# Performance work log

Hardware: AMD Instinct MI355X
Metric: run time of the kernel (lower is better)

## Reference

```python
import jax, jax.numpy as jnp
import numpy as np

N = 50000
E = 800000


def setup_inputs() -> dict:
    key = jax.random.key(0)
    ks = jax.random.split(key, 12)
    d, pd, h, md, od = 64, 3, 128, 64, 64

    def glorot(k, shape):
        fan_in = shape[0]
        return jax.random.normal(k, shape, dtype=jnp.float32) / jnp.sqrt(jnp.float32(fan_in))

    return {
        "x": jax.random.normal(ks[0], (N, d), dtype=jnp.float32),
        "pos": jax.random.normal(ks[1], (N, pd), dtype=jnp.float32),
        "edge_index": jax.random.randint(ks[2], (2, E), 0, N, dtype=jnp.int64 if jax.config.jax_enable_x64 else jnp.int32),
        "W1": glorot(ks[3], (2 * d + pd, h)),
        "b1": jnp.zeros((h,), dtype=jnp.float32),
        "W2": glorot(ks[4], (h, md)),
        "b2": jnp.zeros((md,), dtype=jnp.float32),
        "W3": glorot(ks[5], (d + md, h)),
        "b3": jnp.zeros((h,), dtype=jnp.float32),
        "W4": glorot(ks[6], (h, od)),
        "b4": jnp.zeros((od,), dtype=jnp.float32),
    }


def reference(x, pos, edge_index, W1, b1, W2, b2, W3, b3, W4, b4):
    # flow='target_to_source': i = edge_index[0] (aggregation node), j = edge_index[1]
    idx_i = edge_index[0]
    idx_j = edge_index[1]

    x_i = x[idx_i]          # [E, d]
    x_j = x[idx_j]          # [E, d]
    rel_pos = pos[idx_j] - pos[idx_i]  # [E, pd]  (neighbor_loc='position')

    # message MLP
    msg_in = jnp.concatenate([x_i, x_j - x_i, rel_pos], axis=1)  # [E, 2d+pd]
    hmsg = jax.nn.relu(msg_in @ W1 + b1)
    msg = hmsg @ W2 + b2  # [E, md]

    # scatter-mean aggregation at node i
    num_nodes = x.shape[0]
    summed = jax.ops.segment_sum(msg, idx_i, num_segments=num_nodes)  # [N, md]
    counts = jax.ops.segment_sum(jnp.ones((msg.shape[0],), dtype=msg.dtype), idx_i, num_segments=num_nodes)
    aggr = summed / jnp.maximum(counts, 1.0)[:, None]

    # update MLP (self_val=True: concat own features)
    upd_in = jnp.concatenate([x, aggr], axis=1)  # [N, d+md]
    hupd = jax.nn.relu(upd_in @ W3 + b3)
    return hupd @ W4 + b4  # [N, od]
```

## Files before the change

### kernel.cpp

```cpp
#include <hip/hip_runtime.h>


#define EPB 128
#define NPB 64

typedef __attribute__((ext_vector_type(8))) short bf16x8;
typedef __attribute__((ext_vector_type(4))) float f32x4;

static __device__ __forceinline__ unsigned short f2bf(float f) {
    union { float f; unsigned u; } v; v.f = f;
    unsigned u = v.u + 0x7FFFu + ((v.u >> 16) & 1u);
    return (unsigned short)(u >> 16);
}
static __device__ __forceinline__ float bf2f(unsigned short h) {
    union { unsigned u; float f; } v; v.u = ((unsigned)h) << 16;
    return v.f;
}


__global__ __launch_bounds__(256) void count_kernel(
    const int* __restrict__ ei0, int* __restrict__ cnt, int E)
{
    int e = blockIdx.x * 256 + threadIdx.x;
    if (e < E) atomicAdd(&cnt[ei0[e]], 1);
}

__global__ __launch_bounds__(1024) void scanA_kernel(
    const int* __restrict__ cnt, int* __restrict__ bsum, int N)
{
    __shared__ int ws[16];
    const int i = blockIdx.x * 1024 + threadIdx.x;
    int v = (i < N) ? cnt[i] : 0;
    #pragma unroll
    for (int d = 32; d >= 1; d >>= 1) v += __shfl_down(v, d, 64);
    if ((threadIdx.x & 63) == 0) ws[threadIdx.x >> 6] = v;
    __syncthreads();
    if (threadIdx.x == 0) {
        int s = 0;
        #pragma unroll
        for (int k = 0; k < 16; ++k) s += ws[k];
        bsum[blockIdx.x] = s;
    }
}

__global__ __launch_bounds__(1024) void scanC_kernel(
    const int* __restrict__ cnt, const int* __restrict__ bsum,
    int* __restrict__ off, int N, int Etot)
{
    __shared__ int wsum[16];
    __shared__ int boffs;
    const int i = blockIdx.x * 1024 + threadIdx.x;
    const int lane = threadIdx.x & 63, w = threadIdx.x >> 6;
    if (threadIdx.x < 64) {
        int acc = 0;
        for (int k = threadIdx.x; k < blockIdx.x; k += 64) acc += bsum[k];
        #pragma unroll
        for (int d = 32; d >= 1; d >>= 1) acc += __shfl_down(acc, d, 64);
        if (threadIdx.x == 0) boffs = acc;
    }
    const int v = (i < N) ? cnt[i] : 0;
    int incl = v;
    #pragma unroll
    for (int d = 1; d < 64; d <<= 1) {
        int t = __shfl_up(incl, d, 64);
        if (lane >= d) incl += t;
    }
    if (lane == 63) wsum[w] = incl;
    __syncthreads();
    int pre = 0;
    for (int k = 0; k < w; ++k) pre += wsum[k];
    if (i < N) off[i] = boffs + pre + incl - v;
    if (blockIdx.x == 0 && threadIdx.x == 0) off[N] = Etot;
}

__global__ __launch_bounds__(256) void fill_kernel(
    const int* __restrict__ ei0, const int* __restrict__ ei1,
    const int* __restrict__ off, int* __restrict__ cur,
    int2* __restrict__ eij, int E)
{
    int e = blockIdx.x * 256 + threadIdx.x;
    if (e < E) {
        const int i = ei0[e];
        const int p = atomicAdd(&cur[i], 1);
        int2 v; v.x = i; v.y = ei1[e];
        eij[off[i] + p] = v;
    }
}


__global__ __launch_bounds__(64) void pack_weights_kernel(
    const float* __restrict__ W1, const float* __restrict__ W2,
    const float* __restrict__ W3, const float* __restrict__ W4,
    unsigned short* __restrict__ Wcp, unsigned short* __restrict__ W2p,
    unsigned short* __restrict__ W3p, unsigned short* __restrict__ W4p)
{
    int f = blockIdx.x;
    const int lane = threadIdx.x;
    if (f < 48) {
        const int nt = f / 3, ks = f % 3;
        const int n  = nt * 16 + (lane & 15);
        const int k0 = ks * 32 + (lane >> 4) * 8;
        unsigned short* dst = Wcp + (size_t)f * 512 + lane * 8;
        #pragma unroll
        for (int j = 0; j < 8; ++j) {
            const int k = k0 + j;
            float v = 0.f;
            if (n < 128) {
                if (k < 64)       v = W1[(size_t)k * 128 + n] - W1[(size_t)(64 + k) * 128 + n];
                else if (k < 67)  v = -W1[(size_t)(128 + k - 64) * 128 + n];
            } else {
                const int nq = n - 128;
                if (k < 64)       v = W1[(size_t)(64 + k) * 128 + nq];
                else if (k < 67)  v = W1[(size_t)(128 + k - 64) * 128 + nq];
            }
            dst[j] = f2bf(v);
        }
        return;
    }
    const float* W; unsigned short* out; int K, N, KS;
    if (f < 64)      { W = W2; out = W2p; K = 128; N = 64;  KS = 4; f -= 48; }
    else if (f < 96) { W = W3; out = W3p; K = 128; N = 128; KS = 4; f -= 64; }
    else             { W = W4; out = W4p; K = 128; N = 64;  KS = 4; f -= 96; }
    const int nt = f / KS, ks = f % KS;
    const int n  = nt * 16 + (lane & 15);
    const int k0 = ks * 32 + (lane >> 4) * 8;
    unsigned short* dst = out + (size_t)f * 512 + lane * 8;
    #pragma unroll
    for (int j = 0; j < 8; ++j) {
        float v = (k0 + j < K) ? W[(size_t)(k0 + j) * N + n] : 0.f;
        dst[j] = f2bf(v);
    }
}


__global__ __launch_bounds__(256) void pq_kernel(
    const float* __restrict__ x, const float* __restrict__ pos,
    const unsigned short* __restrict__ Wcp, const float* __restrict__ b1,
    unsigned short* __restrict__ P, unsigned short* __restrict__ Q, int N)
{
    __shared__ unsigned short s[NPB][104];

    const int tid  = threadIdx.x;
    const int wv   = tid >> 6;
    const int lane = tid & 63;
    const int r    = lane >> 4;
    const int c    = lane & 15;
    const int base = blockIdx.x * NPB;

    for (int nl = wv; nl < NPB; nl += 4) {
        const int n = base + nl;
        s[nl][lane] = (n < N) ? f2bf(x[(size_t)n * 64 + lane]) : 0;
        if (lane < 32)
            s[nl][64 + lane] = (n < N && lane < 3) ? f2bf(pos[(size_t)n * 3 + lane]) : 0;
    }
    __syncthreads();

    bf16x8 a[3];
    #pragma unroll
    for (int ks = 0; ks < 3; ++ks)
        a[ks] = *(const bf16x8*)&s[wv * 16 + c][ks * 32 + r * 8];

    f32x4 acc[16];
    #pragma unroll
    for (int nt = 0; nt < 16; ++nt) {
        const float bv = (nt < 8) ? b1[nt * 16 + c] : 0.f;
        acc[nt] = (f32x4){bv, bv, bv, bv};
    }
    #pragma unroll
    for (int nt = 0; nt < 16; ++nt)
        #pragma unroll
        for (int ks = 0; ks < 3; ++ks) {
            const bf16x8 b = *(const bf16x8*)(Wcp + (size_t)(nt * 3 + ks) * 512 + lane * 8);
            acc[nt] = __builtin_amdgcn_mfma_f32_16x16x32_bf16(a[ks], b, acc[nt], 0, 0, 0);
        }

    #pragma unroll
    for (int nt = 0; nt < 16; ++nt)
        #pragma unroll
        for (int reg = 0; reg < 4; ++reg) {
            const int n = base + wv * 16 + r * 4 + reg;
            if (n < N) {
                if (nt < 8) P[(size_t)n * 128 + nt * 16 + c]       = f2bf(acc[nt][reg]);
                else        Q[(size_t)n * 128 + (nt - 8) * 16 + c] = f2bf(acc[nt][reg]);
            }
        }
}


__global__ __launch_bounds__(256) void edge_aggr_mfma(
    const unsigned short* __restrict__ P, const unsigned short* __restrict__ Q,
    const int2* __restrict__ eij,
    const unsigned short* __restrict__ W2p, const float* __restrict__ b2,
    float* __restrict__ aggr, int E)
{
    __shared__ unsigned short s_m[EPB][72];
    __shared__ int2 s_ij[EPB];
    __shared__ int  s_start[EPB + 4];
    __shared__ int  s_wsumA[2];
    __shared__ int  s_nruns;

    const int tid  = threadIdx.x;
    const int wv   = tid >> 6;
    const int lane = tid & 63;
    const int r    = lane >> 4;
    const int c    = lane & 15;
    const int base = blockIdx.x * EPB;
    const int ne   = min(EPB, E - base);

    if (tid < EPB) {
        const int p = base + tid;
        int2 v; v.x = -1; v.y = -1;
        if (p < E) v = eij[p];
        s_ij[tid] = v;
    }
    __syncthreads();

    bf16x8 a2[2][4];
    #pragma unroll
    for (int mh = 0; mh < 2; ++mh) {
        const int2 ij = s_ij[wv * 32 + mh * 16 + c];
        if (ij.x >= 0) {
            const unsigned short* Pi = P + (size_t)ij.x * 128;
            const unsigned short* Qj = Q + (size_t)ij.y * 128;
            #pragma unroll
            for (int ks = 0; ks < 4; ++ks) {
                const bf16x8 pp = *(const bf16x8*)(Pi + ks * 32 + r * 8);
                const bf16x8 qq = *(const bf16x8*)(Qj + ks * 32 + r * 8);
                bf16x8 h;
                #pragma unroll
                for (int t = 0; t < 8; ++t) {
                    const float v = bf2f((unsigned short)pp[t]) + bf2f((unsigned short)qq[t]);
                    h[t] = (short)f2bf(fmaxf(v, 0.f));
                }
                a2[mh][ks] = h;
            }
        } else {
            #pragma unroll
            for (int ks = 0; ks < 4; ++ks) a2[mh][ks] = (bf16x8){0,0,0,0,0,0,0,0};
        }
    }

    f32x4 acc2[2][4];
    #pragma unroll
    for (int nt = 0; nt < 4; ++nt) {
        const float bv = b2[nt * 16 + c];
        acc2[0][nt] = (f32x4){bv, bv, bv, bv};
        acc2[1][nt] = (f32x4){bv, bv, bv, bv};
    }
    #pragma unroll
    for (int nt = 0; nt < 4; ++nt)
        #pragma unroll
        for (int ks = 0; ks < 4; ++ks) {
            const bf16x8 b = *(const bf16x8*)(W2p + (size_t)(nt * 4 + ks) * 512 + lane * 8);
            acc2[0][nt] = __builtin_amdgcn_mfma_f32_16x16x32_bf16(a2[0][ks], b, acc2[0][nt], 0, 0, 0);
            acc2[1][nt] = __builtin_amdgcn_mfma_f32_16x16x32_bf16(a2[1][ks], b, acc2[1][nt], 0, 0, 0);
        }

    #pragma unroll
    for (int mh = 0; mh < 2; ++mh)
        #pragma unroll
        for (int nt = 0; nt < 4; ++nt)
            #pragma unroll
            for (int reg = 0; reg < 4; ++reg) {
                const int row = wv * 32 + mh * 16 + r * 4 + reg;
                s_m[row][nt * 16 + c] = f2bf(acc2[mh][nt][reg]);
            }

    int flag = 0, incl = 0;
    if (tid < EPB) {
        flag = (tid < ne) && (tid == 0 || s_ij[tid].x != s_ij[tid - 1].x);
        incl = flag;
    }
    #pragma unroll
    for (int d = 1; d < 64; d <<= 1) {
        int t = __shfl_up(incl, d, 64);
        if (lane >= d) incl += t;
    }
    if (tid < EPB && lane == 63) s_wsumA[tid >> 6] = incl;
    __syncthreads();
    if (tid < EPB) {
        const int rid = incl + ((tid >= 64) ? s_wsumA[0] : 0);
        if (flag) s_start[rid - 1] = tid;
    }
    if (tid == 0) {
        const int nr = s_wsumA[0] + s_wsumA[1];
        s_nruns = nr;
        s_start[nr] = ne;
    }
    __syncthreads();

    for (int rn = wv; rn < s_nruns; rn += 4) {
        const int e0 = s_start[rn], e1 = s_start[rn + 1];
        const int i  = s_ij[e0].x;
        float acc = 0.f;
        for (int e = e0; e < e1; ++e)
            acc += bf2f(s_m[e][lane]);
        atomicAdd(&aggr[(size_t)i * 64 + lane], acc);
    }
}


__global__ __launch_bounds__(256) void node_mlp_mfma(
    const float* __restrict__ x, const float* __restrict__ aggr,
    const int* __restrict__ off,
    const unsigned short* __restrict__ W3p, const float* __restrict__ b3,
    const unsigned short* __restrict__ W4p, const float* __restrict__ b4,
    float* __restrict__ out, int N)
{
    __shared__ unsigned short s_a[NPB][136];

    const int tid  = threadIdx.x;
    const int wv   = tid >> 6;
    const int lane = tid & 63;
    const int r    = lane >> 4;
    const int c    = lane & 15;
    const int base = blockIdx.x * NPB;

    for (int nl = wv; nl < NPB; nl += 4) {
        const int n = base + nl;
        if (n < N) {
            s_a[nl][lane] = f2bf(x[(size_t)n * 64 + lane]);
            const int deg = off[n + 1] - off[n];
            const float a = aggr[(size_t)n * 64 + lane] / (float)max(deg, 1);
            s_a[nl][64 + lane] = f2bf(a);
        } else {
            s_a[nl][lane] = 0;
            s_a[nl][64 + lane] = 0;
        }
    }
    __syncthreads();

    bf16x8 a1[4];
    #pragma unroll
    for (int ks = 0; ks < 4; ++ks)
        a1[ks] = *(const bf16x8*)&s_a[wv * 16 + c][ks * 32 + r * 8];
    __syncthreads();

    f32x4 acc1[8];
    #pragma unroll
    for (int nt = 0; nt < 8; ++nt) {
        const float bv = b3[nt * 16 + c];
        acc1[nt] = (f32x4){bv, bv, bv, bv};
    }
    #pragma unroll
    for (int nt = 0; nt < 8; ++nt)
        #pragma unroll
        for (int ks = 0; ks < 4; ++ks) {
            const bf16x8 b = *(const bf16x8*)(W3p + (size_t)(nt * 4 + ks) * 512 + lane * 8);
            acc1[nt] = __builtin_amdgcn_mfma_f32_16x16x32_bf16(a1[ks], b, acc1[nt], 0, 0, 0);
        }
    #pragma unroll
    for (int nt = 0; nt < 8; ++nt)
        #pragma unroll
        for (int reg = 0; reg < 4; ++reg)
            s_a[wv * 16 + r * 4 + reg][nt * 16 + c] = f2bf(fmaxf(acc1[nt][reg], 0.f));
    __syncthreads();

    bf16x8 a2[4];
    #pragma unroll
    for (int ks = 0; ks < 4; ++ks)
        a2[ks] = *(const bf16x8*)&s_a[wv * 16 + c][ks * 32 + r * 8];
    __syncthreads();

    f32x4 acc2[4];
    #pragma unroll
    for (int nt = 0; nt < 4; ++nt) {
        const float bv = b4[nt * 16 + c];
        acc2[nt] = (f32x4){bv, bv, bv, bv};
    }
    #pragma unroll
    for (int nt = 0; nt < 4; ++nt)
        #pragma unroll
        for (int ks = 0; ks < 4; ++ks) {
            const bf16x8 b = *(const bf16x8*)(W4p + (size_t)(nt * 4 + ks) * 512 + lane * 8);
            acc2[nt] = __builtin_amdgcn_mfma_f32_16x16x32_bf16(a2[ks], b, acc2[nt], 0, 0, 0);
        }

    #pragma unroll
    for (int nt = 0; nt < 4; ++nt)
        #pragma unroll
        for (int reg = 0; reg < 4; ++reg) {
            float* row = (float*)&s_a[wv * 16 + r * 4 + reg][0];
            row[nt * 16 + c] = acc2[nt][reg];
        }
    __syncthreads();

    {
        const int nl = tid >> 2, q = tid & 3;
        const int n = base + nl;
        if (n < N) {
            const float4* src = (const float4*)((const float*)&s_a[nl][0] + q * 16);
            float4* dst = (float4*)(out + (size_t)n * 64 + q * 16);
            #pragma unroll
            for (int u = 0; u < 4; ++u) dst[u] = src[u];
        }
    }
}


#define EB 32
#define NB 32

__global__ __launch_bounds__(256) void mpnn_edge_atomic_kernel(
    const float* __restrict__ x, const float* __restrict__ pos,
    const int* __restrict__ ei0, const int* __restrict__ ei1,
    const float* __restrict__ W1, const float* __restrict__ b1,
    const float* __restrict__ W2, const float* __restrict__ b2,
    float* __restrict__ summed, float* __restrict__ counts, int E)
{
    __shared__ float s_in[EB][132];
    __shared__ int   s_idx[EB];

    const int tid  = threadIdx.x;
    const int base = blockIdx.x * EB;
    const int wv   = tid >> 6;
    const int lane = tid & 63;

    for (int e = wv; e < EB; e += 4) {
        const int ei = base + e;
        if (ei < E) {
            const int i = ei0[ei];
            const int j = ei1[ei];
            const float xi = x[(size_t)i * 64 + lane];
            const float xj = x[(size_t)j * 64 + lane];
            s_in[e][lane]      = xi;
            s_in[e][64 + lane] = xj - xi;
            if (lane < 3)
                s_in[e][128 + lane] = pos[(size_t)j * 3 + lane] - pos[(size_t)i * 3 + lane];
            if (lane == 0) s_idx[e] = i;
        } else {
            s_in[e][lane] = 0.f; s_in[e][64 + lane] = 0.f;
            if (lane < 3) s_in[e][128 + lane] = 0.f;
            if (lane == 0) s_idx[e] = -1;
        }
    }
    __syncthreads();

    float acc1[4][4];
    {
        const int cg = tid & 31;
        const int er = tid >> 5;
        const float4 bb = *(const float4*)(b1 + 4 * cg);
        #pragma unroll
        for (int t = 0; t < 4; ++t) {
            acc1[t][0] = bb.x; acc1[t][1] = bb.y; acc1[t][2] = bb.z; acc1[t][3] = bb.w;
        }
        for (int k = 0; k < 128; k += 4) {
            float wv4[4][4];
            #pragma unroll
            for (int kk = 0; kk < 4; ++kk) {
                const float4 w = *(const float4*)(W1 + (size_t)(k + kk) * 128 + 4 * cg);
                wv4[kk][0] = w.x; wv4[kk][1] = w.y; wv4[kk][2] = w.z; wv4[kk][3] = w.w;
            }
            #pragma unroll
            for (int t = 0; t < 4; ++t) {
                const float4 m = *(const float4*)(&s_in[er + 8 * t][k]);
                const float mm[4] = {m.x, m.y, m.z, m.w};
                #pragma unroll
                for (int kk = 0; kk < 4; ++kk)
                    #pragma unroll
                    for (int cc = 0; cc < 4; ++cc)
                        acc1[t][cc] += mm[kk] * wv4[kk][cc];
            }
        }
        for (int k = 128; k < 131; ++k) {
            float wk[4];
            #pragma unroll
            for (int cc = 0; cc < 4; ++cc) wk[cc] = W1[(size_t)k * 128 + 4 * cg + cc];
            #pragma unroll
            for (int t = 0; t < 4; ++t) {
                const float m = s_in[er + 8 * t][k];
                #pragma unroll
                for (int cc = 0; cc < 4; ++cc) acc1[t][cc] += m * wk[cc];
            }
        }
    }
    __syncthreads();
    {
        const int cg = tid & 31;
        const int er = tid >> 5;
        #pragma unroll
        for (int t = 0; t < 4; ++t)
            #pragma unroll
            for (int cc = 0; cc < 4; ++cc)
                s_in[er + 8 * t][4 * cg + cc] = fmaxf(acc1[t][cc], 0.f);
    }
    __syncthreads();
    {
        const int cg = tid & 15;
        const int er = tid >> 4;
        float acc[2][4];
        const float4 bb = *(const float4*)(b2 + 4 * cg);
        #pragma unroll
        for (int t = 0; t < 2; ++t) {
            acc[t][0] = bb.x; acc[t][1] = bb.y; acc[t][2] = bb.z; acc[t][3] = bb.w;
        }
        for (int k = 0; k < 128; k += 4) {
            float wv4[4][4];
            #pragma unroll
            for (int kk = 0; kk < 4; ++kk) {
                const float4 w = *(const float4*)(W2 + (size_t)(k + kk) * 64 + 4 * cg);
                wv4[kk][0] = w.x; wv4[kk][1] = w.y; wv4[kk][2] = w.z; wv4[kk][3] = w.w;
            }
            #pragma unroll
            for (int t = 0; t < 2; ++t) {
                const float4 m = *(const float4*)(&s_in[er + 16 * t][k]);
                const float mm[4] = {m.x, m.y, m.z, m.w};
                #pragma unroll
                for (int kk = 0; kk < 4; ++kk)
                    #pragma unroll
                    for (int cc = 0; cc < 4; ++cc)
                        acc[t][cc] += mm[kk] * wv4[kk][cc];
            }
        }
        #pragma unroll
        for (int t = 0; t < 2; ++t) {
            const int e = er + 16 * t;
            const int i = s_idx[e];
            if (i >= 0) {
                #pragma unroll
                for (int cc = 0; cc < 4; ++cc)
                    atomicAdd(&summed[(size_t)i * 64 + 4 * cg + cc], acc[t][cc]);
            }
        }
    }
    if (tid < EB) {
        const int i = s_idx[tid];
        if (i >= 0) atomicAdd(&counts[i], 1.0f);
    }
}

__global__ __launch_bounds__(256) void mpnn_node_legacy_kernel(
    const float* __restrict__ x, const float* __restrict__ summed,
    const float* __restrict__ counts,
    const float* __restrict__ W3, const float* __restrict__ b3,
    const float* __restrict__ W4, const float* __restrict__ b4,
    float* __restrict__ out, int N)
{
    __shared__ float s_in[NB][132];

    const int tid  = threadIdx.x;
    const int base = blockIdx.x * NB;
    const int wv   = tid >> 6;
    const int lane = tid & 63;

    for (int nl = wv; nl < NB; nl += 4) {
        const int n = base + nl;
        if (n < N) {
            s_in[nl][lane] = x[(size_t)n * 64 + lane];
            const float inv = 1.0f / fmaxf(counts[n], 1.0f);
            s_in[nl][64 + lane] = summed[(size_t)n * 64 + lane] * inv;
        } else {
            s_in[nl][lane] = 0.f; s_in[nl][64 + lane] = 0.f;
        }
    }
    __syncthreads();

    float acc1[4][4];
    {
        const int cg = tid & 31;
        const int er = tid >> 5;
        const float4 bb = *(const float4*)(b3 + 4 * cg);
        #pragma unroll
        for (int t = 0; t < 4; ++t) {
            acc1[t][0] = bb.x; acc1[t][1] = bb.y; acc1[t][2] = bb.z; acc1[t][3] = bb.w;
        }
        for (int k = 0; k < 128; k += 4) {
            float wv4[4][4];
            #pragma unroll
            for (int kk = 0; kk < 4; ++kk) {
                const float4 w = *(const float4*)(W3 + (size_t)(k + kk) * 128 + 4 * cg);
                wv4[kk][0] = w.x; wv4[kk][1] = w.y; wv4[kk][2] = w.z; wv4[kk][3] = w.w;
            }
            #pragma unroll
            for (int t = 0; t < 4; ++t) {
                const float4 m = *(const float4*)(&s_in[er + 8 * t][k]);
                const float mm[4] = {m.x, m.y, m.z, m.w};
                #pragma unroll
                for (int kk = 0; kk < 4; ++kk)
                    #pragma unroll
                    for (int cc = 0; cc < 4; ++cc)
                        acc1[t][cc] += mm[kk] * wv4[kk][cc];
            }
        }
    }
    __syncthreads();
    {
        const int cg = tid & 31;
        const int er = tid >> 5;
        #pragma unroll
        for (int t = 0; t < 4; ++t)
            #pragma unroll
            for (int cc = 0; cc < 4; ++cc)
                s_in[er + 8 * t][4 * cg + cc] = fmaxf(acc1[t][cc], 0.f);
    }
    __syncthreads();
    {
        const int cg = tid & 15;
        const int er = tid >> 4;
        float acc[2][4];
        const float4 bb = *(const float4*)(b4 + 4 * cg);
        #pragma unroll
        for (int t = 0; t < 2; ++t) {
            acc[t][0] = bb.x; acc[t][1] = bb.y; acc[t][2] = bb.z; acc[t][3] = bb.w;
        }
        for (int k = 0; k < 128; k += 4) {
            float wv4[4][4];
            #pragma unroll
            for (int kk = 0; kk < 4; ++kk) {
                const float4 w = *(const float4*)(W4 + (size_t)(k + kk) * 64 + 4 * cg);
                wv4[kk][0] = w.x; wv4[kk][1] = w.y; wv4[kk][2] = w.z; wv4[kk][3] = w.w;
            }
            #pragma unroll
            for (int t = 0; t < 2; ++t) {
                const float4 m = *(const float4*)(&s_in[er + 16 * t][k]);
                const float mm[4] = {m.x, m.y, m.z, m.w};
                #pragma unroll
                for (int kk = 0; kk < 4; ++kk)
                    #pragma unroll
                    for (int cc = 0; cc < 4; ++cc)
                        acc[t][cc] += mm[kk] * wv4[kk][cc];
            }
        }
        #pragma unroll
        for (int t = 0; t < 2; ++t) {
            const int n = base + er + 16 * t;
            if (n < N) {
                float4 o;
                o.x = acc[t][0]; o.y = acc[t][1]; o.z = acc[t][2]; o.w = acc[t][3];
                *(float4*)(out + (size_t)n * 64 + 4 * cg) = o;
            }
        }
    }
}


static inline size_t rup(size_t v) { return (v + 255) & ~(size_t)255; }

extern "C" void kernel_launch(void* const* d_in, const int* in_sizes, int n_in,
                              void* d_out, int out_size, void* d_ws, size_t ws_size,
                              hipStream_t stream) {
    const float* x    = (const float*)d_in[0];
    const float* pos  = (const float*)d_in[1];
    const int*   eidx = (const int*)d_in[2];
    const float* W1   = (const float*)d_in[3];
    const float* b1   = (const float*)d_in[4];
    const float* W2   = (const float*)d_in[5];
    const float* b2   = (const float*)d_in[6];
    const float* W3   = (const float*)d_in[7];
    const float* b3   = (const float*)d_in[8];
    const float* W4   = (const float*)d_in[9];
    const float* b4   = (const float*)d_in[10];

    const int N = in_sizes[0] / 64;
    const int E = in_sizes[2] / 2;
    const int* ei0 = eidx;
    const int* ei1 = eidx + E;
    const int nb = (N + 1023) / 1024;

    const size_t p_b    = rup((size_t)N * 128 * 2);
    const size_t q_b    = rup((size_t)N * 128 * 2);
    const size_t wcp_b  = rup(48 * 512 * 2);
    const size_t w2p_b  = rup(16 * 512 * 2);
    const size_t w3p_b  = rup(32 * 512 * 2);
    const size_t w4p_b  = rup(16 * 512 * 2);
    const size_t aggr_b = rup((size_t)N * 64 * 4);
    const size_t cnt_b  = rup((size_t)N * 4);
    const size_t off_b  = rup((size_t)(N + 1) * 4);
    const size_t bsum_b = rup(256 * 4);
    const size_t eij_b  = rup((size_t)E * 8);
    const size_t need = p_b + q_b + wcp_b + w2p_b + w3p_b + w4p_b +
                        aggr_b + 2 * cnt_b + off_b + bsum_b + eij_b;

    if (ws_size >= need) {
        char* p = (char*)d_ws;
        unsigned short* P   = (unsigned short*)p;  p += p_b;
        unsigned short* Q   = (unsigned short*)p;  p += q_b;
        unsigned short* Wcp = (unsigned short*)p;  p += wcp_b;
        unsigned short* W2p = (unsigned short*)p;  p += w2p_b;
        unsigned short* W3p = (unsigned short*)p;  p += w3p_b;
        unsigned short* W4p = (unsigned short*)p;  p += w4p_b;
        float* aggr = (float*)p;  p += aggr_b;
        int* cnt  = (int*)p;  p += cnt_b;
        int* cur  = (int*)p;  p += cnt_b;
        int* off  = (int*)p;  p += off_b;
        int* bsum = (int*)p;  p += bsum_b;
        int2* eij = (int2*)p;

        hipMemsetAsync(aggr, 0, aggr_b + 2 * cnt_b, stream);

        pack_weights_kernel<<<112, 64, 0, stream>>>(W1, W2, W3, W4, Wcp, W2p, W3p, W4p);
        pq_kernel<<<(N + NPB - 1) / NPB, 256, 0, stream>>>(x, pos, Wcp, b1, P, Q, N);

        const int eb256 = (E + 255) / 256;
        count_kernel<<<eb256, 256, 0, stream>>>(ei0, cnt, E);
        scanA_kernel<<<nb, 1024, 0, stream>>>(cnt, bsum, N);
        scanC_kernel<<<nb, 1024, 0, stream>>>(cnt, bsum, off, N, E);
        fill_kernel<<<eb256, 256, 0, stream>>>(ei0, ei1, off, cur, eij, E);

        edge_aggr_mfma<<<(E + EPB - 1) / EPB, 256, 0, stream>>>(
            P, Q, eij, W2p, b2, aggr, E);

        node_mlp_mfma<<<(N + NPB - 1) / NPB, 256, 0, stream>>>(
            x, aggr, off, W3p, b3, W4p, b4, (float*)d_out, N);
    } else {
        float* summed = (float*)d_ws;
        float* counts = summed + (size_t)N * 64;
        hipMemsetAsync(d_ws, 0, ((size_t)N * 64 + N) * sizeof(float), stream);

        mpnn_edge_atomic_kernel<<<(E + EB - 1) / EB, 256, 0, stream>>>(
            x, pos, ei0, ei1, W1, b1, W2, b2, summed, counts, E);
        mpnn_node_legacy_kernel<<<(N + NB - 1) / NB, 256, 0, stream>>>(
            x, summed, counts, W3, b3, W4, b4, (float*)d_out, N);
    }
}
```

Measured before the change: 292.0 us.

## Reuse count-atomic rank in fill, stage P/Q stores via LDS, pack relu-add

The count kernel now keeps the per-edge return value of its atomic as a rank, so the fill kernel no longer needs a second atomic pass or the cur array. The pq kernel stages its P and Q outputs through shared memory so each row is written with coalesced 8-byte stores instead of scattered 2-byte stores. The edge kernel computes the bf16 add plus relu on packed 32-bit pairs with bit masks instead of converting each element separately. In exchange it adds an E-sized rank buffer and extra barriers in the pq kernel.

```diff
diff --git a/kernel.cpp b/kernel.cpp
--- a/kernel.cpp
+++ b/kernel.cpp
@@ -16,13 +16,22 @@
     union { unsigned u; float f; } v; v.u = ((unsigned)h) << 16;
     return v.f;
 }
+static __device__ __forceinline__ unsigned relu_add_pk(unsigned pu, unsigned qu) {
+    union { unsigned u; float f; } plo, phi, qlo, qhi, lo, hi;
+    plo.u = pu << 16;           phi.u = pu & 0xffff0000u;
+    qlo.u = qu << 16;           qhi.u = qu & 0xffff0000u;
+    lo.f = fmaxf(plo.f + qlo.f, 0.f);
+    hi.f = fmaxf(phi.f + qhi.f, 0.f);
+    return (hi.u & 0xffff0000u) | (lo.u >> 16);
+}
 
 
 __global__ __launch_bounds__(256) void count_kernel(
-    const int* __restrict__ ei0, int* __restrict__ cnt, int E)
+    const int* __restrict__ ei0, int* __restrict__ cnt,
+    int* __restrict__ rank, int E)
 {
     int e = blockIdx.x * 256 + threadIdx.x;
-    if (e < E) atomicAdd(&cnt[ei0[e]], 1);
+    if (e < E) rank[e] = atomicAdd(&cnt[ei0[e]], 1);
 }
 
 __global__ __launch_bounds__(1024) void scanA_kernel(
@@ -75,15 +84,14 @@
 
 __global__ __launch_bounds__(256) void fill_kernel(
     const int* __restrict__ ei0, const int* __restrict__ ei1,
-    const int* __restrict__ off, int* __restrict__ cur,
+    const int* __restrict__ off, const int* __restrict__ rank,
     int2* __restrict__ eij, int E)
 {
     int e = blockIdx.x * 256 + threadIdx.x;
     if (e < E) {
         const int i = ei0[e];
-        const int p = atomicAdd(&cur[i], 1);
         int2 v; v.x = i; v.y = ei1[e];
-        eij[off[i] + p] = v;
+        eij[off[i] + rank[e]] = v;
     }
 }
 
@@ -138,7 +146,7 @@
     const unsigned short* __restrict__ Wcp, const float* __restrict__ b1,
     unsigned short* __restrict__ P, unsigned short* __restrict__ Q, int N)
 {
-    __shared__ unsigned short s[NPB][104];
+    __shared__ unsigned short s[NPB][136];
 
     const int tid  = threadIdx.x;
     const int wv   = tid >> 6;
@@ -159,6 +167,7 @@
     #pragma unroll
     for (int ks = 0; ks < 3; ++ks)
         a[ks] = *(const bf16x8*)&s[wv * 16 + c][ks * 32 + r * 8];
+    __syncthreads();
 
     f32x4 acc[16];
     #pragma unroll
@@ -175,15 +184,39 @@
         }
 
     #pragma unroll
-    for (int nt = 0; nt < 16; ++nt)
-        #pragma unroll
-        for (int reg = 0; reg < 4; ++reg) {
-            const int n = base + wv * 16 + r * 4 + reg;
-            if (n < N) {
-                if (nt < 8) P[(size_t)n * 128 + nt * 16 + c]       = f2bf(acc[nt][reg]);
-                else        Q[(size_t)n * 128 + (nt - 8) * 16 + c] = f2bf(acc[nt][reg]);
-            }
-        }
+    for (int nt = 0; nt < 8; ++nt)
+        #pragma unroll
+        for (int reg = 0; reg < 4; ++reg)
+            s[wv * 16 + r * 4 + reg][nt * 16 + c] = f2bf(acc[nt][reg]);
+    __syncthreads();
+    {
+        const int nl = tid >> 2, q = tid & 3;
+        const int n = base + nl;
+        if (n < N) {
+            const ushort4* src = (const ushort4*)&s[nl][0];
+            ushort4* dst = (ushort4*)(P + (size_t)n * 128);
+            #pragma unroll
+            for (int u = 0; u < 8; ++u) dst[q * 8 + u] = src[q * 8 + u];
+        }
+    }
+    __syncthreads();
+
+    #pragma unroll
+    for (int nt = 8; nt < 16; ++nt)
+        #pragma unroll
+        for (int reg = 0; reg < 4; ++reg)
+            s[wv * 16 + r * 4 + reg][(nt - 8) * 16 + c] = f2bf(acc[nt][reg]);
+    __syncthreads();
+    {
+        const int nl = tid >> 2, q = tid & 3;
+        const int n = base + nl;
+        if (n < N) {
+            const ushort4* src = (const ushort4*)&s[nl][0];
+            ushort4* dst = (ushort4*)(Q + (size_t)n * 128);
+            #pragma unroll
+            for (int u = 0; u < 8; ++u) dst[q * 8 + u] = src[q * 8 + u];
+        }
+    }
 }
 
 
@@ -220,19 +253,18 @@
     for (int mh = 0; mh < 2; ++mh) {
         const int2 ij = s_ij[wv * 32 + mh * 16 + c];
         if (ij.x >= 0) {
-            const unsigned short* Pi = P + (size_t)ij.x * 128;
-            const unsigned short* Qj = Q + (size_t)ij.y * 128;
+            const unsigned* Pi = (const unsigned*)(P + (size_t)ij.x * 128);
+            const unsigned* Qj = (const unsigned*)(Q + (size_t)ij.y * 128);
             #pragma unroll
             for (int ks = 0; ks < 4; ++ks) {
-                const bf16x8 pp = *(const bf16x8*)(Pi + ks * 32 + r * 8);
-                const bf16x8 qq = *(const bf16x8*)(Qj + ks * 32 + r * 8);
-                bf16x8 h;
-                #pragma unroll
-                for (int t = 0; t < 8; ++t) {
-                    const float v = bf2f((unsigned short)pp[t]) + bf2f((unsigned short)qq[t]);
-                    h[t] = (short)f2bf(fmaxf(v, 0.f));
-                }
-                a2[mh][ks] = h;
+                const uint4 pu = *(const uint4*)(Pi + ks * 16 + r * 4);
+                const uint4 qu = *(const uint4*)(Qj + ks * 16 + r * 4);
+                uint4 h;
+                h.x = relu_add_pk(pu.x, qu.x);
+                h.y = relu_add_pk(pu.y, qu.y);
+                h.z = relu_add_pk(pu.z, qu.z);
+                h.w = relu_add_pk(pu.w, qu.w);
+                a2[mh][ks] = *(const bf16x8*)&h;
             }
         } else {
             #pragma unroll
@@ -668,9 +700,10 @@
     const size_t cnt_b  = rup((size_t)N * 4);
     const size_t off_b  = rup((size_t)(N + 1) * 4);
     const size_t bsum_b = rup(256 * 4);
+    const size_t rank_b = rup((size_t)E * 4);
     const size_t eij_b  = rup((size_t)E * 8);
     const size_t need = p_b + q_b + wcp_b + w2p_b + w3p_b + w4p_b +
-                        aggr_b + 2 * cnt_b + off_b + bsum_b + eij_b;
+                        aggr_b + cnt_b + off_b + bsum_b + rank_b + eij_b;
 
     if (ws_size >= need) {
         char* p = (char*)d_ws;
@@ -682,21 +715,21 @@
         unsigned short* W4p = (unsigned short*)p;  p += w4p_b;
         float* aggr = (float*)p;  p += aggr_b;
         int* cnt  = (int*)p;  p += cnt_b;
-        int* cur  = (int*)p;  p += cnt_b;
         int* off  = (int*)p;  p += off_b;
         int* bsum = (int*)p;  p += bsum_b;
+        int* rank = (int*)p;  p += rank_b;
         int2* eij = (int2*)p;
 
-        hipMemsetAsync(aggr, 0, aggr_b + 2 * cnt_b, stream);
+        hipMemsetAsync(aggr, 0, aggr_b + cnt_b, stream);
 
         pack_weights_kernel<<<112, 64, 0, stream>>>(W1, W2, W3, W4, Wcp, W2p, W3p, W4p);
         pq_kernel<<<(N + NPB - 1) / NPB, 256, 0, stream>>>(x, pos, Wcp, b1, P, Q, N);
 
         const int eb256 = (E + 255) / 256;
-        count_kernel<<<eb256, 256, 0, stream>>>(ei0, cnt, E);
+        count_kernel<<<eb256, 256, 0, stream>>>(ei0, cnt, rank, E);
         scanA_kernel<<<nb, 1024, 0, stream>>>(cnt, bsum, N);
         scanC_kernel<<<nb, 1024, 0, stream>>>(cnt, bsum, off, N, E);
-        fill_kernel<<<eb256, 256, 0, stream>>>(ei0, ei1, off, cur, eij, E);
+        fill_kernel<<<eb256, 256, 0, stream>>>(ei0, ei1, off, rank, eij, E);
 
         edge_aggr_mfma<<<(E + EPB - 1) / EPB, 256, 0, stream>>>(
             P, Q, eij, W2p, b2, aggr, E);
```

After: 262.2 us. 10.2% less time.
